# Kernel optimization log

Measured on AMD Instinct MI355X. Metric: run time of the kernel, lower is better.

Reference implementation:

```python
import jax, jax.numpy as jnp
import numpy as np

WS = 7      # window size
SS = 3      # shift size
NH = 6      # num heads
C = 192     # dim
B = 32
HH = 112
WW = 112


def _rel_pos_index(ws):
    coords = np.stack(np.meshgrid(np.arange(ws), np.arange(ws), indexing='ij'))
    cf = coords.reshape(2, -1)
    rel = (cf[:, :, None] - cf[:, None, :]).transpose(1, 2, 0)
    rel[:, :, 0] += ws - 1
    rel[:, :, 1] += ws - 1
    rel[:, :, 0] *= 2 * ws - 1
    return rel.sum(-1)  # (N, N) int


def _attn_mask(H, W, ws, ss):
    # standard Swin SW-MSA mask: -100 where tokens come from different regions
    img = np.zeros((H, W))
    cnt = 0
    for h in (slice(0, -ws), slice(-ws, -ss), slice(-ss, None)):
        for w in (slice(0, -ws), slice(-ws, -ss), slice(-ss, None)):
            img[h, w] = cnt
            cnt += 1
    mw = img.reshape(H // ws, ws, W // ws, ws).transpose(0, 2, 1, 3).reshape(-1, ws * ws)
    diff = mw[:, None, :] - mw[:, :, None]
    return np.where(diff != 0, -100.0, 0.0).astype(np.float32)  # (nW, N, N)


def _ln(x, g, b, eps=1e-5):
    m = x.mean(-1, keepdims=True)
    v = ((x - m) ** 2).mean(-1, keepdims=True)
    return (x - m) * jax.lax.rsqrt(v + eps) * g + b


def setup_inputs() -> dict:
    key = jax.random.key(0)
    ks = jax.random.split(key, 8)
    hid = 4 * C
    nbias = (2 * WS - 1) * (2 * WS - 1)
    return {
        'x': jax.random.normal(ks[0], (B, HH * WW, C), dtype=jnp.float32),
        'norm1_g': jnp.ones((C,), jnp.float32),
        'norm1_b': jnp.zeros((C,), jnp.float32),
        'qkv_w': jax.random.normal(ks[1], (3 * C, C), jnp.float32) * 0.02,
        'qkv_b': jnp.zeros((3 * C,), jnp.float32),
        'rpb_table': jax.random.normal(ks[2], (nbias, NH), jnp.float32) * 0.02,
        'proj_w': jax.random.normal(ks[3], (C, C), jnp.float32) * 0.02,
        'proj_b': jnp.zeros((C,), jnp.float32),
        'norm2_g': jnp.ones((C,), jnp.float32),
        'norm2_b': jnp.zeros((C,), jnp.float32),
        'fc1_w': jax.random.normal(ks[4], (hid, C), jnp.float32) * 0.02,
        'fc1_b': jnp.zeros((hid,), jnp.float32),
        'fc2_w': jax.random.normal(ks[5], (C, hid), jnp.float32) * 0.02,
        'fc2_b': jnp.zeros((C,), jnp.float32),
        'H': HH,
        'W': WW,
    }


def reference(x, norm1_g, norm1_b, qkv_w, qkv_b, rpb_table, proj_w, proj_b,
              norm2_g, norm2_b, fc1_w, fc1_b, fc2_w, fc2_b, H, W):
    Bb, L, Cc = x.shape
    N = WS * WS
    hd = Cc // NH
    rpi = jnp.asarray(_rel_pos_index(WS))                      # (N, N)
    amask = jnp.asarray(_attn_mask(H, W, WS, SS))              # (nW, N, N)
    nW = amask.shape[0]

    shortcut = x
    h = _ln(x, norm1_g, norm1_b).reshape(Bb, H, W, Cc)
    # cyclic shift
    h = jnp.roll(h, shift=(-SS, -SS), axis=(1, 2))
    # window partition -> (B*nW, N, C)
    h = h.reshape(Bb, H // WS, WS, W // WS, WS, Cc).transpose(0, 1, 3, 2, 4, 5)
    xw = h.reshape(-1, N, Cc)
    Bn = xw.shape[0]

    qkv = (xw @ qkv_w.T + qkv_b).reshape(Bn, N, 3, NH, hd).transpose(2, 0, 3, 1, 4)
    q, k, v = qkv[0], qkv[1], qkv[2]                           # (Bn, NH, N, hd)
    q = q * (hd ** -0.5)
    attn = jnp.einsum('bhnd,bhmd->bhnm', q, k)                 # (Bn, NH, N, N)
    bias = rpb_table[rpi.reshape(-1)].reshape(N, N, NH).transpose(2, 0, 1)
    attn = attn + bias[None]
    attn = (attn.reshape(Bb, nW, NH, N, N) + amask[None, :, None]).reshape(Bn, NH, N, N)
    attn = jax.nn.softmax(attn, axis=-1)
    out = jnp.einsum('bhnm,bhmd->bhnd', attn, v).transpose(0, 2, 1, 3).reshape(Bn, N, Cc)
    out = out @ proj_w.T + proj_b

    # window reverse + reverse cyclic shift
    out = out.reshape(Bb, H // WS, W // WS, WS, WS, Cc).transpose(0, 1, 3, 2, 4, 5).reshape(Bb, H, W, Cc)
    out = jnp.roll(out, shift=(SS, SS), axis=(1, 2)).reshape(Bb, L, Cc)

    x = shortcut + out
    y = _ln(x, norm2_g, norm2_b)
    y = jax.nn.gelu(y @ fc1_w.T + fc1_b, approximate=False) @ fc2_w.T + fc2_b
    return x + y
```

## Files before the change

### kernel.cpp

```cpp
#include <hip/hip_runtime.h>
#include <stdint.h>
#include <math.h>


typedef unsigned short u16;
typedef unsigned int   u32;
typedef __bf16 v8bf __attribute__((ext_vector_type(8)));
typedef float  v4f  __attribute__((ext_vector_type(4)));
typedef u16    v8u16 __attribute__((ext_vector_type(8)));
typedef u16    v4u16 __attribute__((ext_vector_type(4)));

#define MFMA16(a,b,c) __builtin_amdgcn_mfma_f32_16x16x32_bf16(a,b,c,0,0,0)

#define QSC  0.17677669529663687f

__device__ __forceinline__ u16 f2bf(float f){
  return __builtin_bit_cast(u16, (__bf16)f);
}

__device__ __forceinline__ void async16(void* lds, const void* g){
  __builtin_amdgcn_global_load_lds(
      (__attribute__((address_space(1))) void*)(g),
      (__attribute__((address_space(3))) void*)(lds), 16, 0, 0);
}

__global__ __launch_bounds__(256)
void convw(const float* __restrict__ s0, const float* __restrict__ s1,
           const float* __restrict__ s2, const float* __restrict__ s3,
           u16* __restrict__ d){
  int i = blockIdx.x * 256 + threadIdx.x;
  float v;
  if (i < 110592){
    v = s0[i];
    if (i < 36864) v *= QSC;
  }
  else if (i < 147456)  v = s1[i - 110592];
  else if (i < 294912)  v = s2[i - 147456];
  else                  v = s3[i - 294912];
  d[i] = f2bf(v);
}

__global__ __launch_bounds__(256)
void bmt_k(const float* __restrict__ rpb, float* __restrict__ bmt){
  int idx = blockIdx.x * 256 + threadIdx.x;
  int r  = idx & 3, lg = (idx >> 2) & 3, lr = (idx >> 4) & 15;
  int n  = (idx >> 8) & 3, m = (idx >> 10) & 3;
  int t  = idx >> 12; int h = t % 6, cls = t / 6;
  int row = m*16 + lg*4 + r, col = n*16 + lr;
  float v;
  if (row >= 49 || col >= 49){
    v = -1e30f;
  } else {
    int i1 = row / 7, j1 = row - i1 * 7;
    int i2 = col / 7, j2 = col - i2 * 7;
    int ridx = (i1 - i2 + 6) * 13 + (j1 - j2 + 6);
    v = rpb[ridx * 6 + h];
    int lh1 = (cls & 2) ? (i1 < 4 ? 1 : 2) : 0;
    int lw1 = (cls & 1) ? (j1 < 4 ? 1 : 2) : 0;
    int lh2 = (cls & 2) ? (i2 < 4 ? 1 : 2) : 0;
    int lw2 = (cls & 1) ? (j2 < 4 ? 1 : 2) : 0;
    if (lh1 * 3 + lw1 != lh2 * 3 + lw2) v -= 100.f;
  }
  bmt[idx] = v;
}

template<bool GATHER>
__global__ __launch_bounds__(256)
void ln_kern(const float* __restrict__ x, const float* __restrict__ g,
             const float* __restrict__ b, u16* __restrict__ o){
  const int ts  = threadIdx.x >> 4;
  const int l16 = threadIdx.x & 15;
  const int r   = blockIdx.x * 16 + ts;
  const float* src;
  if (GATHER){
    u32 wdx = (u32)r / 49u; int nn = r - (int)wdx * 49;
    int bb = (int)(wdx >> 8); int wl = (int)(wdx & 255);
    int wh = wl >> 4, wwi = wl & 15;
    int ii = (int)((u32)nn / 7u), jj = nn - ii * 7;
    int th = wh * 7 + ii + 3;  if (th >= 112) th -= 112;
    int tw = wwi * 7 + jj + 3; if (tw >= 112) tw -= 112;
    src = x + (u32)(bb * 12544 + th * 112 + tw) * 192u;
  } else {
    src = x + (u32)r * 192u;
  }
  const float4 a0 = *(const float4*)(src + l16*12);
  const float4 a1 = *(const float4*)(src + l16*12 + 4);
  const float4 a2 = *(const float4*)(src + l16*12 + 8);
  float sm = ((a0.x+a0.y)+(a0.z+a0.w)) + ((a1.x+a1.y)+(a1.z+a1.w))
           + ((a2.x+a2.y)+(a2.z+a2.w));
  float sq = ((a0.x*a0.x+a0.y*a0.y)+(a0.z*a0.z+a0.w*a0.w))
           + ((a1.x*a1.x+a1.y*a1.y)+(a1.z*a1.z+a1.w*a1.w))
           + ((a2.x*a2.x+a2.y*a2.y)+(a2.z*a2.z+a2.w*a2.w));
  #pragma unroll
  for (int d = 1; d < 16; d <<= 1){
    sm += __shfl_xor(sm, d, 64);
    sq += __shfl_xor(sq, d, 64);
  }
  float mean = sm * (1.f/192.f);
  float var  = sq * (1.f/192.f) - mean * mean;
  float rs   = rsqrtf(var + 1e-5f);
  const float4 g0 = *(const float4*)(g + l16*12);
  const float4 g1 = *(const float4*)(g + l16*12 + 4);
  const float4 g2 = *(const float4*)(g + l16*12 + 8);
  const float4 b0 = *(const float4*)(b + l16*12);
  const float4 b1 = *(const float4*)(b + l16*12 + 4);
  const float4 b2 = *(const float4*)(b + l16*12 + 8);
  u16* dst = o + (u32)r * 192u + l16 * 12;
  v4u16 w0, w1, w2;
  w0[0]=f2bf((a0.x-mean)*rs*g0.x+b0.x); w0[1]=f2bf((a0.y-mean)*rs*g0.y+b0.y);
  w0[2]=f2bf((a0.z-mean)*rs*g0.z+b0.z); w0[3]=f2bf((a0.w-mean)*rs*g0.w+b0.w);
  w1[0]=f2bf((a1.x-mean)*rs*g1.x+b1.x); w1[1]=f2bf((a1.y-mean)*rs*g1.y+b1.y);
  w1[2]=f2bf((a1.z-mean)*rs*g1.z+b1.z); w1[3]=f2bf((a1.w-mean)*rs*g1.w+b1.w);
  w2[0]=f2bf((a2.x-mean)*rs*g2.x+b2.x); w2[1]=f2bf((a2.y-mean)*rs*g2.y+b2.y);
  w2[2]=f2bf((a2.z-mean)*rs*g2.z+b2.z); w2[3]=f2bf((a2.w-mean)*rs*g2.w+b2.w);
  *(v4u16*)(dst)     = w0;
  *(v4u16*)(dst + 4) = w1;
  *(v4u16*)(dst + 8) = w2;
}

template<int EPI, int LDA, int LDW>
__global__ __launch_bounds__(512)
void gemm_bt(const u16* __restrict__ A, int aRowOff,
             const u16* __restrict__ W, int K, int ncol,
             const float* __restrict__ bias,
             u16* __restrict__ ob, float* __restrict__ of,
             const float* __restrict__ xres, int oRowOff, u32 hstr){
  constexpr bool TRN = (EPI == 0);
  __shared__ __align__(16) u16 sA[128 * 200];
  __shared__ __align__(16) u16 sW[64 * 200];
  const int tid = threadIdx.x;
  const int wv = tid >> 6, lnn = tid & 63;
  const int lr = lnn & 15, lg = lnn >> 4;
  const int win = 56 * ncol;
  const int grp = (int)blockIdx.x / win, loc = (int)blockIdx.x - grp * win;
  const int rloc = loc % 56, cblk = loc / 56;
  const int m0   = (grp * 56 + rloc) * 128;
  const int col0 = cblk * 64;
  const int wr = wv >> 1, wc = wv & 1;

  const int c0   = col0 + wc*32 + lr;
  const int chb0 = col0 + wc*32 + lg*4;
  const int chb1 = chb0 + 16;

  v4f acc[2][2];
  if (TRN){
    float4 bv0 = *(const float4*)&bias[chb0];
    float4 bv1 = *(const float4*)&bias[chb1];
    if (chb0 < 192){ bv0.x*=QSC; bv0.y*=QSC; bv0.z*=QSC; bv0.w*=QSC; }
    if (chb1 < 192){ bv1.x*=QSC; bv1.y*=QSC; bv1.z*=QSC; bv1.w*=QSC; }
    acc[0][0] = acc[0][1] = (v4f){bv0.x, bv0.y, bv0.z, bv0.w};
    acc[1][0] = acc[1][1] = (v4f){bv1.x, bv1.y, bv1.z, bv1.w};
  } else {
    const float b0v = bias[c0];
    const float b1v = bias[c0 + 16];
    #pragma unroll
    for (int m = 0; m < 2; ++m){
      acc[m][0] = (v4f){b0v, b0v, b0v, b0v};
      acc[m][1] = (v4f){b1v, b1v, b1v, b1v};
    }
  }

  const int rA0 = (int)((u32)tid / 25u);
  const int cA0 = tid - rA0 * 25;
  const u32 aBase = (u32)(aRowOff + m0);
  const int nK = K / 192;
  for (int ks = 0; ks < nK; ++ks){
    if (ks) __syncthreads();
    const int k0 = ks * 192;
    int ra = rA0, ca = cA0;
    #pragma unroll
    for (int it = 0; it < 6; ++it){
      int cc = (ca == 24) ? 23 : ca;
      async16((char*)sA + (size_t)(it * 512 + wv * 64) * 16,
              A + (aBase + (u32)ra) * (u32)LDA + (u32)(k0 + cc * 8));
      ra += 20; ca += 12; if (ca >= 25){ ca -= 25; ra += 1; }
    }
    if (tid < 128){
      int cc = (ca == 24) ? 23 : ca;
      async16((char*)sA + (size_t)(3072 + wv * 64) * 16,
              A + (aBase + (u32)ra) * (u32)LDA + (u32)(k0 + cc * 8));
    }
    int rw = rA0, cw = cA0;
    #pragma unroll
    for (int it = 0; it < 3; ++it){
      int cc = (cw == 24) ? 23 : cw;
      async16((char*)sW + (size_t)(it * 512 + wv * 64) * 16,
              W + (u32)(col0 + rw) * (u32)LDW + (u32)(k0 + cc * 8));
      rw += 20; cw += 12; if (cw >= 25){ cw -= 25; rw += 1; }
    }
    if (tid < 64){
      int cc = (cw == 24) ? 23 : cw;
      async16((char*)sW + (size_t)1536 * 16,
              W + (u32)(col0 + rw) * (u32)LDW + (u32)(k0 + cc * 8));
    }
    __syncthreads();

    #pragma unroll
    for (int kk = 0; kk < 6; ++kk){
      v8bf af[2], wf[2];
      #pragma unroll
      for (int m = 0; m < 2; ++m)
        af[m] = *(const v8bf*)&sA[(wr*32 + m*16 + lr) * 200 + kk*32 + lg*8];
      #pragma unroll
      for (int n = 0; n < 2; ++n)
        wf[n] = *(const v8bf*)&sW[(wc*32 + n*16 + lr) * 200 + kk*32 + lg*8];
      if (TRN){
        #pragma unroll
        for (int n = 0; n < 2; ++n)
          #pragma unroll
          for (int m = 0; m < 2; ++m)
            acc[n][m] = MFMA16(wf[n], af[m], acc[n][m]);
      } else {
        #pragma unroll
        for (int m = 0; m < 2; ++m)
          #pragma unroll
          for (int n = 0; n < 2; ++n)
            acc[m][n] = MFMA16(af[m], wf[n], acc[m][n]);
      }
    }
  }

  if (EPI == 0){
    u32 chpart[2];
    const int chbs[2] = {chb0, chb1};
    #pragma unroll
    for (int n = 0; n < 2; ++n){
      int ch = chbs[n];
      int which = (ch >= 384) ? 2 : ((ch >= 192) ? 1 : 0);
      int rem = ch - which * 192;
      chpart[n] = (u32)which * hstr + (u32)((rem >> 5) * 1568 + (rem & 31));
    }
    #pragma unroll
    for (int m = 0; m < 2; ++m){
      const int t = m0 + wr*32 + m*16 + lr;
      u32 wdx = (u32)t / 49u; u32 tnn = (u32)t - wdx * 49u;
      const u32 rowpart = wdx * 9408u + tnn * 32u;
      #pragma unroll
      for (int n = 0; n < 2; ++n){
        v4u16 pk;
        pk[0] = f2bf(acc[n][m][0]); pk[1] = f2bf(acc[n][m][1]);
        pk[2] = f2bf(acc[n][m][2]); pk[3] = f2bf(acc[n][m][3]);
        *(v4u16*)&ob[chpart[n] + rowpart] = pk;
      }
    }
  } else if (EPI == 1){
    #pragma unroll
    for (int m = 0; m < 2; ++m){
      #pragma unroll
      for (int r = 0; r < 4; ++r){
        const int gr = m0 + wr*32 + m*16 + lg*4 + r;
        u32 wdx = (u32)gr / 49u; int nn = gr - (int)wdx * 49;
        int bb = (int)(wdx >> 8); int wl = (int)(wdx & 255);
        int wh = wl >> 4, wwi = wl & 15;
        int ii = (int)((u32)nn / 7u), jj = nn - ii * 7;
        int th = wh * 7 + ii + 3;  if (th >= 112) th -= 112;
        int tw = wwi * 7 + jj + 3; if (tw >= 112) tw -= 112;
        u32 adr = (u32)(bb * 12544 + th * 112 + tw) * 192u + (u32)c0;
        of[adr]      = xres[adr]      + acc[m][0][r];
        of[adr + 16] = xres[adr + 16] + acc[m][1][r];
      }
    }
  } else if (EPI == 3){
    #pragma unroll
    for (int m = 0; m < 2; ++m){
      #pragma unroll
      for (int r = 0; r < 4; ++r){
        const u32 adr = (u32)(oRowOff + m0 + wr*32 + m*16 + lg*4 + r) * 192u
                        + (u32)c0;
        of[adr]      += acc[m][0][r];
        of[adr + 16] += acc[m][1][r];
      }
    }
  } else {
    #pragma unroll
    for (int m = 0; m < 2; ++m){
      #pragma unroll
      for (int r = 0; r < 4; ++r){
        const u32 base = (u32)(m0 + wr*32 + m*16 + lg*4 + r) * 768u + (u32)c0;
        float v0 = acc[m][0][r], v1 = acc[m][1][r];
        ob[base]      = f2bf(0.5f * v0 * (1.0f + erff(v0 * 0.7071067811865475f)));
        ob[base + 16] = f2bf(0.5f * v1 * (1.0f + erff(v1 * 0.7071067811865475f)));
      }
    }
  }
}

__global__ __launch_bounds__(256, 4)
void attn_k(const u16* __restrict__ qkv, const float* __restrict__ bmt,
            u16* __restrict__ aout, u32 wOff, u32 hstr){
  __shared__ __align__(16) u16 plds[4][64 * 64];
  const int wv = threadIdx.x >> 6, lnn = threadIdx.x & 63;
  const int lr = lnn & 15, lg = lnn >> 4;
  const u32 gid = (u32)blockIdx.x * 4u + (u32)wv;
  const u32 w = gid / 6u; const int h = (int)(gid - w * 6u);
  const u16* qb = qkv + (size_t)gid * 1568;
  const u16* kb = qb + hstr;
  const u16* vb = kb + hstr;
  const u32 wg = w + wOff;

  const int wl = (int)(wg & 255u);
  const int cls = (((wl >> 4) == 15) ? 2 : 0) | (((wl & 15) == 15) ? 1 : 0);
  const float* bmv = bmt + ((u32)(cls * 6 + h) << 12);
  v4f s[4][4];
  #pragma unroll
  for (int m = 0; m < 4; ++m)
    #pragma unroll
    for (int n = 0; n < 4; ++n)
      s[m][n] = *(const v4f*)&bmv[(u32)(((m*4 + n)*16 + lr)*16 + lg*4)];

  v8bf aq[4], bk4[4];
  #pragma unroll
  for (int m = 0; m < 4; ++m) aq[m]  = *(const v8bf*)(qb + (m*16 + lr)*32 + lg*8);
  #pragma unroll
  for (int n = 0; n < 4; ++n) bk4[n] = *(const v8bf*)(kb + (n*16 + lr)*32 + lg*8);
  #pragma unroll
  for (int m = 0; m < 4; ++m)
    #pragma unroll
    for (int n = 0; n < 4; ++n) s[m][n] = MFMA16(aq[m], bk4[n], s[m][n]);

  v8u16 bvu[2][2];
  #pragma unroll
  for (int n2 = 0; n2 < 2; ++n2)
    #pragma unroll
    for (int ksi = 0; ksi < 2; ++ksi)
      #pragma unroll
      for (int e = 0; e < 8; ++e){
        int kp = ksi * 32 + lg * 8 + e;
        int t  = (kp >> 2) + (kp & 3) * 16;
        bvu[n2][ksi][e] = vb[(u32)(t * 32 + n2 * 16 + lr)];
      }

  #pragma unroll
  for (int m = 0; m < 4; ++m)
    #pragma unroll
    for (int r = 0; r < 4; ++r){
      int row = m*16 + lg*4 + r;
      v4u16 pk;
      pk[0] = f2bf(__expf(s[m][0][r]));
      pk[1] = f2bf(__expf(s[m][1][r]));
      pk[2] = f2bf(__expf(s[m][2][r]));
      pk[3] = f2bf(__expf(s[m][3][r]));
      *(v4u16*)((char*)&plds[wv][0] + row*128 + ((lr*8) ^ ((row & 7) << 4))) = pk;
    }

  v8bf pa[4][2];
  #pragma unroll
  for (int m2 = 0; m2 < 4; ++m2)
    #pragma unroll
    for (int ksi = 0; ksi < 2; ++ksi){
      int row2 = m2*16 + lr;
      pa[m2][ksi] = *(const v8bf*)((const char*)&plds[wv][0] + row2*128 +
                                   ((ksi*64 + lg*16) ^ ((row2 & 7) << 4)));
    }

  v8u16 onesu;
  #pragma unroll
  for (int e = 0; e < 8; ++e) onesu[e] = (lr == 0) ? (u16)0x3F80 : (u16)0;
  const v8bf onesf = __builtin_bit_cast(v8bf, onesu);

  const v4f zf = {0.f, 0.f, 0.f, 0.f};
  v4f o2[4][2], sacc[4];
  #pragma unroll
  for (int m2 = 0; m2 < 4; ++m2){
    o2[m2][0] = zf; o2[m2][1] = zf; sacc[m2] = zf;
  }
  #pragma unroll
  for (int ksi = 0; ksi < 2; ++ksi)
    #pragma unroll
    for (int m2 = 0; m2 < 4; ++m2){
      o2[m2][0] = MFMA16(pa[m2][ksi], __builtin_bit_cast(v8bf, bvu[0][ksi]), o2[m2][0]);
      o2[m2][1] = MFMA16(pa[m2][ksi], __builtin_bit_cast(v8bf, bvu[1][ksi]), o2[m2][1]);
      sacc[m2]  = MFMA16(pa[m2][ksi], onesf, sacc[m2]);
    }

  float inv[4][4];
  #pragma unroll
  for (int m2 = 0; m2 < 4; ++m2)
    #pragma unroll
    for (int r = 0; r < 4; ++r)
      inv[m2][r] = 1.0f / __shfl(sacc[m2][r], lnn & 48, 64);

  #pragma unroll
  for (int m2 = 0; m2 < 4; ++m2){
    #pragma unroll
    for (int n2 = 0; n2 < 2; ++n2){
      #pragma unroll
      for (int r = 0; r < 4; ++r){
        int row = m2*16 + lg*4 + r;
        if (row < 49){
          float val = o2[m2][n2][r] * inv[m2][r];
          aout[(wg * 49u + (u32)row) * 192u + (u32)(h*32 + n2*16 + lr)] = f2bf(val);
        }
      }
    }
  }
}

extern "C" void kernel_launch(void* const* d_in, const int* in_sizes, int n_in,
                              void* d_out, int out_size, void* d_ws, size_t ws_size,
                              hipStream_t stream){
  const float* x     = (const float*)d_in[0];
  const float* n1g   = (const float*)d_in[1];
  const float* n1b   = (const float*)d_in[2];
  const float* qkvw  = (const float*)d_in[3];
  const float* qkvb  = (const float*)d_in[4];
  const float* rpb   = (const float*)d_in[5];
  const float* projw = (const float*)d_in[6];
  const float* projb = (const float*)d_in[7];
  const float* n2g   = (const float*)d_in[8];
  const float* n2b   = (const float*)d_in[9];
  const float* fc1w  = (const float*)d_in[10];
  const float* fc1b  = (const float*)d_in[11];
  const float* fc2w  = (const float*)d_in[12];
  const float* fc2b  = (const float*)d_in[13];
  float* out = (float*)d_out;

  char* ws  = (char*)d_ws;
  u16* bufA = (u16*)ws;
  u16* bufB = (u16*)(ws + 462422016L);
  u16* wq   = (u16*)(ws + 616562688L);
  u16* wp   = wq + 110592;
  u16* w1   = wp + 36864;
  u16* w2   = w1 + 147456;
  float* bmt = (float*)d_out;

  convw<<<1728, 256, 0, stream>>>(qkvw, projw, fc1w, fc2w, wq);
  bmt_k<<<384, 256, 0, stream>>>(rpb, bmt);

  ln_kern<true><<<25088, 256, 0, stream>>>(x, n1g, n1b, bufB);

  const u32 HC = 9633792u;
  for (int c = 0; c < 8; ++c){
    const int rowOff = c * 50176;
    gemm_bt<0, 192, 192><<<392*9, 512, 0, stream>>>(bufB, rowOff, wq, 192, 9,
                                                    qkvb, bufA, nullptr,
                                                    nullptr, 0, HC);
    attn_k<<<1536, 256, 0, stream>>>(bufA, bmt, bufB, (u32)(c * 1024), HC);
  }

  gemm_bt<1, 192, 192><<<3136*3, 512, 0, stream>>>(bufB, 0, wp, 192, 3,
                                                   projb, nullptr, out, x, 0, 0);
  ln_kern<false><<<25088, 256, 0, stream>>>(out, n2g, n2b, bufB);

  for (int c = 0; c < 8; ++c){
    const int off = c * 50176;
    gemm_bt<2, 192, 192><<<392*12, 512, 0, stream>>>(bufB, off, w1, 192, 12,
                                                     fc1b, bufA, nullptr,
                                                     nullptr, 0, 0);
    gemm_bt<3, 768, 768><<<392*3, 512, 0, stream>>>(bufA, 0, w2, 768, 3,
                                                    fc2b, nullptr, out,
                                                    nullptr, off, 0);
  }
}
```

Measured before the change: 1.349 ms.

## Chunk LayerNorm and projection into per-chunk loops to keep intermediates cache-resident

Moves both LayerNorm passes and the output projection GEMM inside the 8-way row-chunk loops, so each chunk's normalized input, qkv, attention output and MLP hidden live in small workspace buffers. The aim is to shrink the working set so intermediates can stay in the large last-level cache instead of round-tripping full-size buffers through HBM. The bias/mask table moves from the output buffer into the workspace. The cost is more kernel launches, with smaller grids per launch. The attention kernel's output indexing switches from a global window index to a chunk-local one, and the projection epilogue now takes the chunk row offset.

```diff
diff --git a/kernel.cpp b/kernel.cpp
--- a/kernel.cpp
+++ b/kernel.cpp
@@ -67,10 +67,11 @@
 template<bool GATHER>
 __global__ __launch_bounds__(256)
 void ln_kern(const float* __restrict__ x, const float* __restrict__ g,
-             const float* __restrict__ b, u16* __restrict__ o){
+             const float* __restrict__ b, u16* __restrict__ o, int rowOff){
   const int ts  = threadIdx.x >> 4;
   const int l16 = threadIdx.x & 15;
-  const int r   = blockIdx.x * 16 + ts;
+  const int rl  = blockIdx.x * 16 + ts;
+  const int r   = rowOff + rl;
   const float* src;
   if (GATHER){
     u32 wdx = (u32)r / 49u; int nn = r - (int)wdx * 49;
@@ -105,7 +106,7 @@
   const float4 b0 = *(const float4*)(b + l16*12);
   const float4 b1 = *(const float4*)(b + l16*12 + 4);
   const float4 b2 = *(const float4*)(b + l16*12 + 8);
-  u16* dst = o + (u32)r * 192u + l16 * 12;
+  u16* dst = o + (u32)rl * 192u + l16 * 12;
   v4u16 w0, w1, w2;
   w0[0]=f2bf((a0.x-mean)*rs*g0.x+b0.x); w0[1]=f2bf((a0.y-mean)*rs*g0.y+b0.y);
   w0[2]=f2bf((a0.z-mean)*rs*g0.z+b0.z); w0[3]=f2bf((a0.w-mean)*rs*g0.w+b0.w);
@@ -248,7 +249,7 @@
     for (int m = 0; m < 2; ++m){
       #pragma unroll
       for (int r = 0; r < 4; ++r){
-        const int gr = m0 + wr*32 + m*16 + lg*4 + r;
+        const int gr = oRowOff + m0 + wr*32 + m*16 + lg*4 + r;
         u32 wdx = (u32)gr / 49u; int nn = gr - (int)wdx * 49;
         int bb = (int)(wdx >> 8); int wl = (int)(wdx & 255);
         int wh = wl >> 4, wwi = wl & 15;
@@ -389,7 +390,7 @@
         int row = m2*16 + lg*4 + r;
         if (row < 49){
           float val = o2[m2][n2][r] * inv[m2][r];
-          aout[(wg * 49u + (u32)row) * 192u + (u32)(h*32 + n2*16 + lr)] = f2bf(val);
+          aout[(w * 49u + (u32)row) * 192u + (u32)(h*32 + n2*16 + lr)] = f2bf(val);
         }
       }
     }
@@ -415,39 +416,39 @@
   const float* fc2b  = (const float*)d_in[13];
   float* out = (float*)d_out;
 
-  char* ws  = (char*)d_ws;
-  u16* bufA = (u16*)ws;
-  u16* bufB = (u16*)(ws + 462422016L);
-  u16* wq   = (u16*)(ws + 616562688L);
-  u16* wp   = wq + 110592;
-  u16* w1   = wp + 36864;
-  u16* w2   = w1 + 147456;
-  float* bmt = (float*)d_out;
+  char* ws   = (char*)d_ws;
+  u16* bigC  = (u16*)ws;
+  u16* xwC   = (u16*)(ws + 80000000L);
+  u16* aoC   = (u16*)(ws + 100000000L);
+  float* bmt = (float*)(ws + 120000000L);
+  u16* wq    = (u16*)(ws + 121000000L);
+  u16* wp    = wq + 110592;
+  u16* w1    = wp + 36864;
+  u16* w2    = w1 + 147456;
 
   convw<<<1728, 256, 0, stream>>>(qkvw, projw, fc1w, fc2w, wq);
   bmt_k<<<384, 256, 0, stream>>>(rpb, bmt);
-
-  ln_kern<true><<<25088, 256, 0, stream>>>(x, n1g, n1b, bufB);
 
   const u32 HC = 9633792u;
   for (int c = 0; c < 8; ++c){
     const int rowOff = c * 50176;
-    gemm_bt<0, 192, 192><<<392*9, 512, 0, stream>>>(bufB, rowOff, wq, 192, 9,
-                                                    qkvb, bufA, nullptr,
+    ln_kern<true><<<3136, 256, 0, stream>>>(x, n1g, n1b, xwC, rowOff);
+    gemm_bt<0, 192, 192><<<392*9, 512, 0, stream>>>(xwC, 0, wq, 192, 9,
+                                                    qkvb, bigC, nullptr,
                                                     nullptr, 0, HC);
-    attn_k<<<1536, 256, 0, stream>>>(bufA, bmt, bufB, (u32)(c * 1024), HC);
-  }
-
-  gemm_bt<1, 192, 192><<<3136*3, 512, 0, stream>>>(bufB, 0, wp, 192, 3,
-                                                   projb, nullptr, out, x, 0, 0);
-  ln_kern<false><<<25088, 256, 0, stream>>>(out, n2g, n2b, bufB);
+    attn_k<<<1536, 256, 0, stream>>>(bigC, bmt, aoC, (u32)(c * 1024), HC);
+    gemm_bt<1, 192, 192><<<392*3, 512, 0, stream>>>(aoC, 0, wp, 192, 3,
+                                                    projb, nullptr, out,
+                                                    x, rowOff, 0);
+  }
 
   for (int c = 0; c < 8; ++c){
     const int off = c * 50176;
-    gemm_bt<2, 192, 192><<<392*12, 512, 0, stream>>>(bufB, off, w1, 192, 12,
-                                                     fc1b, bufA, nullptr,
+    ln_kern<false><<<3136, 256, 0, stream>>>(out, n2g, n2b, xwC, off);
+    gemm_bt<2, 192, 192><<<392*12, 512, 0, stream>>>(xwC, 0, w1, 192, 12,
+                                                     fc1b, bigC, nullptr,
                                                      nullptr, 0, 0);
-    gemm_bt<3, 768, 768><<<392*3, 512, 0, stream>>>(bufA, 0, w2, 768, 3,
+    gemm_bt<3, 768, 768><<<392*3, 512, 0, stream>>>(bigC, 0, w2, 768, 3,
                                                     fc2b, nullptr, out,
                                                     nullptr, off, 0);
   }
```

Result: faster. 1.304 ms, median of 2 (-3.3%).
